# Performance work log

Hardware: AMD Instinct MI355X
Metric: run time of the kernel (lower is better)

Reference implementation:

```python
import jax, jax.numpy as jnp
import numpy as np

COMMITMENT_COST = 0.25
DECAY = 0.99
EPS = 1e-5
TOP_K = 3


def setup_inputs() -> dict:
    key = jax.random.key(0)
    k1, k2, k3, k4 = jax.random.split(key, 4)
    B, T, D, K = 16, 1024, 256, 4096
    return {
        "inputs": jax.random.normal(k1, (B, T, D), dtype=jnp.float32),
        "embedding_weight": jax.random.normal(k2, (K, D), dtype=jnp.float32),
        "ema_cluster_size": jax.random.uniform(k3, (K,), dtype=jnp.float32),
        "ema_w": jax.random.normal(k4, (K, D), dtype=jnp.float32),
    }


def reference(inputs, embedding_weight, ema_cluster_size, ema_w):
    B, T, D = inputs.shape
    K = embedding_weight.shape[0]
    flat = inputs.reshape(-1, D)  # [N, D], N = B*T
    N = flat.shape[0]

    dists = (jnp.sum(flat * flat, axis=1, keepdims=True)
             + jnp.sum(embedding_weight * embedding_weight, axis=1)
             - 2.0 * (flat @ embedding_weight.T))

    # top-k smallest distances
    _, idx = jax.lax.top_k(-dists, TOP_K)  # [N, k]

    # one-hot scatter encodings [N, K] (k ones per row)
    enc = jnp.zeros((N, K), dtype=flat.dtype).at[jnp.arange(N)[:, None], idx].set(1.0)

    # gather codebook vectors -> [B, T, k, D]
    quant = embedding_weight[idx].reshape(B, T, TOP_K, D)
    inp_rep = jnp.broadcast_to(inputs[:, :, None, :], (B, T, TOP_K, D))

    # EMA codebook update (training path)
    new_cs = ema_cluster_size * DECAY + (1.0 - DECAY) * enc.sum(axis=0)
    n = jnp.sum(new_cs)
    new_cs = (new_cs + EPS) / (n + K * EPS) * n
    dw = enc.T @ flat                                # [K, D]
    new_ema_w = ema_w * DECAY + (1.0 - DECAY) * dw
    updated_embeddings = new_ema_w / new_cs[:, None]

    # commitment loss with straight-through estimator
    e_latent_loss = jnp.mean((jax.lax.stop_gradient(quant) - inp_rep) ** 2)
    loss = COMMITMENT_COST * e_latent_loss
    quant_st = inp_rep + jax.lax.stop_gradient(quant - inp_rep)

    avg_probs = enc.mean(axis=0)
    perplexity = jnp.exp(-jnp.sum(avg_probs * jnp.log(avg_probs + 1e-10)))

    encoding_indices = idx.reshape(B, T, TOP_K)
    distances = dists.reshape(B, T, K)
    return (loss, quant_st, perplexity, avg_probs, encoding_indices, distances,
            new_cs, new_ema_w, updated_embeddings)
```

## Files before the change

### kernel.cpp

```cpp
#include <hip/hip_runtime.h>
#include <hip/hip_bf16.h>
#include <math.h>

#define N_ROWS 16384
#define DIM    256
#define KC     4096
#define TOPK   3
#define KSPLIT 768
#define TOTAL_E (N_ROWS * TOPK)
#define CHUNK 24

#define O_LOSS   0
#define O_QUANT  1
#define O_PERP   12582913
#define O_AVGP   12582914
#define O_IDX    12587010
#define O_DIST   12636162
#define O_NCS    79745026
#define O_NEMAW  79749122
#define O_UPD    80797698

typedef _Float16 h4_t __attribute__((ext_vector_type(4)));
typedef _Float16 h8_t __attribute__((ext_vector_type(8)));
typedef float    f4_t __attribute__((ext_vector_type(4)));

#define GLL(g, l) __builtin_amdgcn_global_load_lds( \
    (const __attribute__((address_space(1))) unsigned int*)(g), \
    (__attribute__((address_space(3))) unsigned int*)(l), 16, 0, 0)

__global__ __launch_bounds__(256) void rownorm_kernel(
    const float* __restrict__ X, float* __restrict__ out, int rows)
{
    int wave = threadIdx.x >> 6;
    int lane = threadIdx.x & 63;
    int row  = blockIdx.x * 4 + wave;
    if (row >= rows) return;
    float4 v = *(const float4*)&X[(size_t)row * DIM + lane * 4];
    float s = v.x*v.x + v.y*v.y + v.z*v.z + v.w*v.w;
    #pragma unroll
    for (int off = 32; off; off >>= 1) s += __shfl_down(s, off);
    if (lane == 0) out[row] = s;
}

__global__ __launch_bounds__(256) void convert_kernel(
    const float* __restrict__ X, _Float16* __restrict__ Q,
    int lo_off, int hi2_off)
{
    int wave = threadIdx.x >> 6;
    int lane = threadIdx.x & 63;
    int row  = blockIdx.x * 4 + wave;
    float4 v = *(const float4*)&X[(size_t)row * DIM + lane * 4];
    h4_t hi, lo;
    hi[0] = (_Float16)v.x; lo[0] = (_Float16)(v.x - (float)hi[0]);
    hi[1] = (_Float16)v.y; lo[1] = (_Float16)(v.y - (float)hi[1]);
    hi[2] = (_Float16)v.z; lo[2] = (_Float16)(v.z - (float)hi[2]);
    hi[3] = (_Float16)v.w; lo[3] = (_Float16)(v.w - (float)hi[3]);
    _Float16* q = Q + (size_t)row * KSPLIT + lane * 4;
    *(h4_t*)(q)           = hi;
    *(h4_t*)(q + hi2_off) = hi;
    *(h4_t*)(q + lo_off)  = lo;
}

__global__ __launch_bounds__(256) void gemm_dist_kernel(
    const _Float16* __restrict__ Aq,
    const _Float16* __restrict__ Bq,
    const float* __restrict__ xn,
    const float* __restrict__ en,
    float* __restrict__ dist)
{
    __shared__ _Float16 As[128 * 64];
    __shared__ _Float16 Bs[128 * 64];

    int bid = blockIdx.x;
    int swz = (bid & 7) * 512 + (bid >> 3);
    int m0 = (swz >> 5) * 128;
    int n0 = (swz & 31) * 128;

    const int tid = threadIdx.x;
    const int w = tid >> 6, l = tid & 63;
    const int wr = w >> 1, wc = w & 1;

    f4_t acc[4][4] = {};

    const int srow = l >> 3;
    const int scol = (l & 7) * 8;
    const _Float16* Abase = Aq + (size_t)m0 * KSPLIT;
    const _Float16* Bbase = Bq + (size_t)n0 * KSPLIT;

    for (int kt = 0; kt < KSPLIT; kt += 64) {
        #pragma unroll
        for (int i = 0; i < 4; i++) {
            int c = w * 4 + i;
            int rg = c * 8 + srow;
            GLL(Abase + (size_t)rg * KSPLIT + kt + scol, &As[c * 512]);
            GLL(Bbase + (size_t)rg * KSPLIT + kt + scol, &Bs[c * 512]);
        }
        __syncthreads();

        #pragma unroll
        for (int ks = 0; ks < 2; ks++) {
            h8_t a[4], b[4];
            #pragma unroll
            for (int mf = 0; mf < 4; mf++)
                a[mf] = *(const h8_t*)&As[(wr*64 + mf*16 + (l & 15)) * 64 + ks*32 + (l >> 4) * 8];
            #pragma unroll
            for (int nf = 0; nf < 4; nf++)
                b[nf] = *(const h8_t*)&Bs[(wc*64 + nf*16 + (l & 15)) * 64 + ks*32 + (l >> 4) * 8];
            #pragma unroll
            for (int mf = 0; mf < 4; mf++)
                #pragma unroll
                for (int nf = 0; nf < 4; nf++)
                    acc[mf][nf] = __builtin_amdgcn_mfma_f32_16x16x32_f16(
                        a[mf], b[nf], acc[mf][nf], 0, 0, 0);
        }
        __syncthreads();
    }

    const int cl = l & 15, rh = l >> 4;
    float ecv[4];
    #pragma unroll
    for (int nf = 0; nf < 4; nf++) ecv[nf] = en[n0 + wc*64 + nf*16 + cl];

    #pragma unroll
    for (int mf = 0; mf < 4; mf++) {
        int r0 = m0 + wr*64 + mf*16 + rh*4;
        float x0 = xn[r0], x1 = xn[r0+1], x2 = xn[r0+2], x3 = xn[r0+3];
        #pragma unroll
        for (int nf = 0; nf < 4; nf++) {
            int c = n0 + wc*64 + nf*16 + cl;
            float* dp = &dist[(size_t)r0 * KC + c];
            dp[0]           = x0 + ecv[nf] - 2.0f * acc[mf][nf][0];
            dp[(size_t)KC]  = x1 + ecv[nf] - 2.0f * acc[mf][nf][1];
            dp[(size_t)KC*2]= x2 + ecv[nf] - 2.0f * acc[mf][nf][2];
            dp[(size_t)KC*3]= x3 + ecv[nf] - 2.0f * acc[mf][nf][3];
        }
    }
}

__device__ __forceinline__ bool vi_lt(float v, int i, float u, int j)
{
    return (v < u) || (v == u && i < j);
}

__global__ __launch_bounds__(256) void top3_kernel(
    const float* __restrict__ dist, int* __restrict__ idxw,
    float* __restrict__ out_idx, float* __restrict__ counts,
    float* __restrict__ loss_part)
{
    __shared__ float blk_loss;
    if (threadIdx.x == 0) blk_loss = 0.0f;
    __syncthreads();

    int wave = threadIdx.x >> 6;
    int lane = threadIdx.x & 63;
    int row  = blockIdx.x * 4 + wave;
    const float* dr = dist + (size_t)row * KC;

    float v0 = INFINITY, v1 = INFINITY, v2 = INFINITY;
    int   i0 = 0x7fffffff, i1 = 0x7fffffff, i2 = 0x7fffffff;

    #pragma unroll 4
    for (int it = 0; it < 16; it++) {
        int c = (it * 64 + lane) * 4;
        float4 d = *(const float4*)&dr[c];
        float dv[4] = {d.x, d.y, d.z, d.w};
        #pragma unroll
        for (int q = 0; q < 4; q++) {
            float v = dv[q]; int ci = c + q;
            if (vi_lt(v, ci, v2, i2)) {
                v2 = v; i2 = ci;
                if (vi_lt(v2, i2, v1, i1)) { float tv = v1; int ti = i1; v1 = v2; i1 = i2; v2 = tv; i2 = ti; }
                if (vi_lt(v1, i1, v0, i0)) { float tv = v0; int ti = i0; v0 = v1; i0 = i1; v1 = tv; i1 = ti; }
            }
        }
    }

    #pragma unroll
    for (int off = 1; off < 64; off <<= 1) {
        float u0 = __shfl_xor(v0, off), u1 = __shfl_xor(v1, off), u2 = __shfl_xor(v2, off);
        int   j0 = __shfl_xor(i0, off), j1 = __shfl_xor(i1, off), j2 = __shfl_xor(i2, off);
        float av[3] = {v0, v1, v2}; int ai[3] = {i0, i1, i2};
        float bv[3] = {u0, u1, u2}; int bi[3] = {j0, j1, j2};
        float rv[3]; int ri[3];
        int p = 0, q = 0;
        #pragma unroll
        for (int t = 0; t < 3; t++) {
            bool ta = vi_lt(av[p], ai[p], bv[q], bi[q]);
            rv[t] = ta ? av[p] : bv[q];
            ri[t] = ta ? ai[p] : bi[q];
            p += ta ? 1 : 0; q += ta ? 0 : 1;
        }
        v0 = rv[0]; v1 = rv[1]; v2 = rv[2];
        i0 = ri[0]; i1 = ri[1]; i2 = ri[2];
    }

    if (lane == 0) {
        int base = row * TOPK;
        idxw[base + 0] = i0; idxw[base + 1] = i1; idxw[base + 2] = i2;
        out_idx[base + 0] = (float)i0;
        out_idx[base + 1] = (float)i1;
        out_idx[base + 2] = (float)i2;
        atomicAdd(&counts[i0], 1.0f);
        atomicAdd(&counts[i1], 1.0f);
        atomicAdd(&counts[i2], 1.0f);
        atomicAdd(&blk_loss, v0 + v1 + v2);
    }
    __syncthreads();
    if (threadIdx.x == 0) loss_part[blockIdx.x] = blk_loss;
}

__global__ __launch_bounds__(256) void quant_copy_kernel(
    const int* __restrict__ idxw, const float* __restrict__ E,
    float* __restrict__ quant_out)
{
    int wave = threadIdx.x >> 6;
    int lane = threadIdx.x & 63;
    int j = blockIdx.x * 4 + wave;
    int code = idxw[j];
    float4 v = *(const float4*)&E[(size_t)code * DIM + lane * 4];
    *(float4*)&quant_out[(size_t)j * DIM + lane * 4] = v;
}

__global__ __launch_bounds__(256) void kstage1_kernel(
    const float* __restrict__ counts, const float* __restrict__ ecs,
    float* __restrict__ avgp, float* __restrict__ scalars)
{
    int k = blockIdx.x * 256 + threadIdx.x;
    float cnt = counts[k];
    float pr = ecs[k] * 0.99f + 0.01f * cnt;
    float p = cnt * (1.0f / (float)N_ROWS);
    avgp[k] = p;
    float ent = p * logf(p + 1e-10f);
    int lane = threadIdx.x & 63;
    #pragma unroll
    for (int off = 32; off; off >>= 1) {
        pr  += __shfl_down(pr, off);
        ent += __shfl_down(ent, off);
    }
    if (lane == 0) {
        atomicAdd(&scalars[0], pr);
        atomicAdd(&scalars[2], ent);
    }
}

__global__ __launch_bounds__(256) void kstage2_kernel(
    const float* __restrict__ counts, const float* __restrict__ ecs,
    const float* __restrict__ scalars, float* __restrict__ ncs)
{
    int k = blockIdx.x * 256 + threadIdx.x;
    float pre = ecs[k] * 0.99f + 0.01f * counts[k];
    float nt = scalars[0];
    ncs[k] = (pre + 1e-5f) / (nt + (float)KC * 1e-5f) * nt;
}

__global__ __launch_bounds__(1024) void scan_kernel(
    const float* __restrict__ counts, int* __restrict__ offsets)
{
    __shared__ int lds[1024];
    int t = threadIdx.x;
    int c[4]; int s = 0;
    #pragma unroll
    for (int q = 0; q < 4; q++) { c[q] = (int)(counts[t * 4 + q] + 0.5f); s += c[q]; }
    lds[t] = s;
    __syncthreads();
    for (int off = 1; off < 1024; off <<= 1) {
        int v = (t >= off) ? lds[t - off] : 0;
        __syncthreads();
        lds[t] += v;
        __syncthreads();
    }
    int base = lds[t] - s;
    offsets[t * 4 + 0] = base;
    offsets[t * 4 + 1] = base + c[0];
    offsets[t * 4 + 2] = base + c[0] + c[1];
    offsets[t * 4 + 3] = base + c[0] + c[1] + c[2];
    if (t == 1023) offsets[4096] = lds[1023];
}

__global__ __launch_bounds__(256) void bucket_fill_kernel(
    const int* __restrict__ idxw, const int* __restrict__ offsets,
    int* __restrict__ fill, int* __restrict__ bucket_list)
{
    int j = blockIdx.x * 256 + threadIdx.x;
    int code = idxw[j];
    int pos = atomicAdd(&fill[code], 1);
    bucket_list[offsets[code] + pos] = (code << 14) | (j / 3);
}

__global__ __launch_bounds__(256) void codeacc_kernel(
    const int* __restrict__ bl, const float* __restrict__ flat,
    float* __restrict__ dw)
{
    int wave = threadIdx.x >> 6;
    int lane = threadIdx.x & 63;
    int chunk = blockIdx.x * 4 + wave;
    int beg = chunk * CHUNK;

    int ent[CHUNK];
    #pragma unroll
    for (int q = 0; q < CHUNK; q++) ent[q] = bl[beg + q];

    float4 acc = {0.0f, 0.0f, 0.0f, 0.0f};
    int prev = ent[0] >> 14;
    #pragma unroll
    for (int q = 0; q < CHUNK; q++) {
        int code = ent[q] >> 14;
        int n    = ent[q] & 0x3fff;
        if (code != prev) {
            float* p = &dw[(size_t)prev * DIM + lane * 4];
            atomicAdd(p + 0, acc.x); atomicAdd(p + 1, acc.y);
            atomicAdd(p + 2, acc.z); atomicAdd(p + 3, acc.w);
            acc.x = acc.y = acc.z = acc.w = 0.0f;
            prev = code;
        }
        float4 v = *(const float4*)&flat[(size_t)n * DIM + lane * 4];
        acc.x += v.x; acc.y += v.y; acc.z += v.z; acc.w += v.w;
    }
    float* p = &dw[(size_t)prev * DIM + lane * 4];
    atomicAdd(p + 0, acc.x); atomicAdd(p + 1, acc.y);
    atomicAdd(p + 2, acc.z); atomicAdd(p + 3, acc.w);
}

__global__ __launch_bounds__(256) void finalize_kernel(
    const float* __restrict__ dw, const float* __restrict__ emaw,
    const float* __restrict__ ncs, float* __restrict__ nemaw,
    float* __restrict__ upd)
{
    int wave = threadIdx.x >> 6;
    int lane = threadIdx.x & 63;
    int k = blockIdx.x * 4 + wave;
    size_t o = (size_t)k * DIM + lane * 4;
    float4 d = *(const float4*)&dw[o];
    float4 w = *(const float4*)&emaw[o];
    float4 nm;
    nm.x = 0.99f * w.x + 0.01f * d.x;
    nm.y = 0.99f * w.y + 0.01f * d.y;
    nm.z = 0.99f * w.z + 0.01f * d.z;
    nm.w = 0.99f * w.w + 0.01f * d.w;
    *(float4*)&nemaw[o] = nm;
    float inv = ncs[k];
    float4 u = {nm.x / inv, nm.y / inv, nm.z / inv, nm.w / inv};
    *(float4*)&upd[o] = u;
}

__global__ __launch_bounds__(1024) void loss_reduce_kernel(
    const float* __restrict__ lp, float* __restrict__ out)
{
    __shared__ float ls[16];
    int t = threadIdx.x;
    float s = lp[t] + lp[t + 1024] + lp[t + 2048] + lp[t + 3072];
    #pragma unroll
    for (int off = 32; off; off >>= 1) s += __shfl_down(s, off);
    if ((t & 63) == 0) ls[t >> 6] = s;
    __syncthreads();
    if (t == 0) {
        float tot = 0.0f;
        #pragma unroll
        for (int i = 0; i < 16; i++) tot += ls[i];
        out[O_LOSS] = 0.25f * tot / (float)(N_ROWS * TOPK * DIM);
    }
}

__global__ void final_kernel(const float* __restrict__ scalars, float* __restrict__ out)
{
    out[O_PERP] = expf(-scalars[2]);
}

extern "C" void kernel_launch(void* const* d_in, const int* in_sizes, int n_in,
                              void* d_out, int out_size, void* d_ws, size_t ws_size,
                              hipStream_t stream)
{
    const float* inputs = (const float*)d_in[0];
    const float* emb    = (const float*)d_in[1];
    const float* ecs    = (const float*)d_in[2];
    const float* emaw   = (const float*)d_in[3];
    float* out = (float*)d_out;
    char* ws = (char*)d_ws;

    int*   idxw        = (int*)ws;
    int*   bucket_list = (int*)(ws + 196608);
    float* counts      = (float*)(ws + 393216);
    int*   offsets     = (int*)(ws + 409600);
    int*   fill        = (int*)(ws + 430080);
    float* xn          = (float*)(ws + 446464);
    float* en          = (float*)(ws + 512000);
    float* scalars     = (float*)(ws + 528384);
    float* loss_part   = (float*)(ws + 528448);

    _Float16* Aq = (_Float16*)(out + 4);
    _Float16* Bq = (_Float16*)(out + 6291464);
    float*    dw = out + 8000000;

    hipMemsetAsync(counts, 0, KC * sizeof(float), stream);
    hipMemsetAsync(fill, 0, KC * sizeof(int), stream);
    hipMemsetAsync(scalars, 0, 8 * sizeof(float), stream);
    hipMemsetAsync(dw, 0, KC * DIM * sizeof(float), stream);

    convert_kernel<<<N_ROWS / 4, 256, 0, stream>>>(inputs, Aq, 512, 256);
    convert_kernel<<<KC / 4, 256, 0, stream>>>(emb, Bq, 256, 512);

    rownorm_kernel<<<N_ROWS / 4, 256, 0, stream>>>(inputs, xn, N_ROWS);
    rownorm_kernel<<<KC / 4, 256, 0, stream>>>(emb, en, KC);

    gemm_dist_kernel<<<(N_ROWS / 128) * (KC / 128), 256, 0, stream>>>(
        Aq, Bq, xn, en, out + O_DIST);

    top3_kernel<<<N_ROWS / 4, 256, 0, stream>>>(
        out + O_DIST, idxw, out + O_IDX, counts, loss_part);

    kstage1_kernel<<<KC / 256, 256, 0, stream>>>(counts, ecs, out + O_AVGP, scalars);
    kstage2_kernel<<<KC / 256, 256, 0, stream>>>(counts, ecs, scalars, out + O_NCS);
    scan_kernel<<<1, 1024, 0, stream>>>(counts, offsets);
    bucket_fill_kernel<<<(N_ROWS * TOPK) / 256, 256, 0, stream>>>(
        idxw, offsets, fill, bucket_list);

    codeacc_kernel<<<(TOTAL_E / CHUNK) / 4, 256, 0, stream>>>(
        bucket_list, inputs, dw);
    finalize_kernel<<<KC / 4, 256, 0, stream>>>(
        dw, emaw, out + O_NCS, out + O_NEMAW, out + O_UPD);

    quant_copy_kernel<<<(N_ROWS * TOPK) / 4, 256, 0, stream>>>(
        idxw, emb, out + O_QUANT);

    loss_reduce_kernel<<<1, 1024, 0, stream>>>(loss_part, out);
    final_kernel<<<1, 1, 0, stream>>>(scalars, out);
}
```

Baseline: 723.6 us.

## Fuse per-tile top-3 selection into distance GEMM epilogue and swizzle LDS

Computes a partial top-3 per row for each 128-column tile inside the GEMM epilogue. Partials are combined through shuffles and LDS, then written to a small partial buffer that a lightweight merge kernel reduces to the final top-3. This removes the full re-read of the 268 MB distance matrix by the old top3 kernel. It also adds an XOR swizzle to the LDS layout to reduce bank conflicts on fragment reads, at the cost of extra epilogue work and a scratch region carved out of the output buffer.

```diff
diff --git a/kernel.cpp b/kernel.cpp
--- a/kernel.cpp
+++ b/kernel.cpp
@@ -27,6 +27,32 @@
 #define GLL(g, l) __builtin_amdgcn_global_load_lds( \
     (const __attribute__((address_space(1))) unsigned int*)(g), \
     (__attribute__((address_space(3))) unsigned int*)(l), 16, 0, 0)
+
+__device__ __forceinline__ bool vi_lt(float v, int i, float u, int j)
+{
+    return (v < u) || (v == u && i < j);
+}
+
+__device__ __forceinline__ void ins3(float v, int i,
+    float& v0, int& i0, float& v1, int& i1, float& v2, int& i2)
+{
+    if (vi_lt(v, i, v2, i2)) {
+        v2 = v; i2 = i;
+        if (vi_lt(v2, i2, v1, i1)) { float tv=v1; int ti=i1; v1=v2; i1=i2; v2=tv; i2=ti; }
+        if (vi_lt(v1, i1, v0, i0)) { float tv=v0; int ti=i0; v0=v1; i0=i1; v1=tv; i1=ti; }
+    }
+}
+
+#define MERGE_SHFL(off) { \
+    float u0=__shfl_xor(v0,off), u1=__shfl_xor(v1,off), u2=__shfl_xor(v2,off); \
+    int   j0=__shfl_xor(i0,off), j1=__shfl_xor(i1,off), j2=__shfl_xor(i2,off); \
+    float av[3]={v0,v1,v2}; int ai[3]={i0,i1,i2}; \
+    float bv[3]={u0,u1,u2}; int bi[3]={j0,j1,j2}; \
+    float rv[3]; int ri[3]; int p=0,q=0; \
+    _Pragma("unroll") \
+    for (int t=0;t<3;t++){ bool ta=vi_lt(av[p],ai[p],bv[q],bi[q]); \
+      rv[t]=ta?av[p]:bv[q]; ri[t]=ta?ai[p]:bi[q]; p+=ta?1:0; q+=ta?0:1; } \
+    v0=rv[0];v1=rv[1];v2=rv[2];i0=ri[0];i1=ri[1];i2=ri[2]; }
 
 __global__ __launch_bounds__(256) void rownorm_kernel(
     const float* __restrict__ X, float* __restrict__ out, int rows)
@@ -66,7 +92,8 @@
     const _Float16* __restrict__ Bq,
     const float* __restrict__ xn,
     const float* __restrict__ en,
-    float* __restrict__ dist)
+    float* __restrict__ dist,
+    float2* __restrict__ part)
 {
     __shared__ _Float16 As[128 * 64];
     __shared__ _Float16 Bs[128 * 64];
@@ -83,7 +110,7 @@
     f4_t acc[4][4] = {};
 
     const int srow = l >> 3;
-    const int scol = (l & 7) * 8;
+    const int scol = ((l & 7) ^ srow) * 8;
     const _Float16* Abase = Aq + (size_t)m0 * KSPLIT;
     const _Float16* Bbase = Bq + (size_t)n0 * KSPLIT;
 
@@ -101,11 +128,17 @@
         for (int ks = 0; ks < 2; ks++) {
             h8_t a[4], b[4];
             #pragma unroll
-            for (int mf = 0; mf < 4; mf++)
-                a[mf] = *(const h8_t*)&As[(wr*64 + mf*16 + (l & 15)) * 64 + ks*32 + (l >> 4) * 8];
+            for (int mf = 0; mf < 4; mf++) {
+                int ra = wr*64 + mf*16 + (l & 15);
+                int ho = (ks*32 + (l >> 4) * 8) ^ ((ra & 7) * 8);
+                a[mf] = *(const h8_t*)&As[ra * 64 + ho];
+            }
             #pragma unroll
-            for (int nf = 0; nf < 4; nf++)
-                b[nf] = *(const h8_t*)&Bs[(wc*64 + nf*16 + (l & 15)) * 64 + ks*32 + (l >> 4) * 8];
+            for (int nf = 0; nf < 4; nf++) {
+                int rb = wc*64 + nf*16 + (l & 15);
+                int ho = (ks*32 + (l >> 4) * 8) ^ ((rb & 7) * 8);
+                b[nf] = *(const h8_t*)&Bs[rb * 64 + ho];
+            }
             #pragma unroll
             for (int mf = 0; mf < 4; mf++)
                 #pragma unroll
@@ -121,29 +154,62 @@
     #pragma unroll
     for (int nf = 0; nf < 4; nf++) ecv[nf] = en[n0 + wc*64 + nf*16 + cl];
 
+    float2* pt = (float2*)As;
+
     #pragma unroll
     for (int mf = 0; mf < 4; mf++) {
         int r0 = m0 + wr*64 + mf*16 + rh*4;
-        float x0 = xn[r0], x1 = xn[r0+1], x2 = xn[r0+2], x3 = xn[r0+3];
+        float xr[4] = {xn[r0], xn[r0+1], xn[r0+2], xn[r0+3]};
+        float dv[4][4];
         #pragma unroll
         for (int nf = 0; nf < 4; nf++) {
             int c = n0 + wc*64 + nf*16 + cl;
             float* dp = &dist[(size_t)r0 * KC + c];
-            dp[0]           = x0 + ecv[nf] - 2.0f * acc[mf][nf][0];
-            dp[(size_t)KC]  = x1 + ecv[nf] - 2.0f * acc[mf][nf][1];
-            dp[(size_t)KC*2]= x2 + ecv[nf] - 2.0f * acc[mf][nf][2];
-            dp[(size_t)KC*3]= x3 + ecv[nf] - 2.0f * acc[mf][nf][3];
+            #pragma unroll
+            for (int rg = 0; rg < 4; rg++) {
+                float d = xr[rg] + ecv[nf] - 2.0f * acc[mf][nf][rg];
+                dv[nf][rg] = d;
+                dp[(size_t)KC * rg] = d;
+            }
         }
-    }
-}
-
-__device__ __forceinline__ bool vi_lt(float v, int i, float u, int j)
-{
-    return (v < u) || (v == u && i < j);
-}
-
-__global__ __launch_bounds__(256) void top3_kernel(
-    const float* __restrict__ dist, int* __restrict__ idxw,
+        #pragma unroll
+        for (int rg = 0; rg < 4; rg++) {
+            float v0=INFINITY, v1=INFINITY, v2=INFINITY;
+            int   i0=0x7fffffff, i1=0x7fffffff, i2=0x7fffffff;
+            #pragma unroll
+            for (int nf = 0; nf < 4; nf++)
+                ins3(dv[nf][rg], n0 + wc*64 + nf*16 + cl, v0,i0,v1,i1,v2,i2);
+            MERGE_SHFL(1); MERGE_SHFL(2); MERGE_SHFL(4); MERGE_SHFL(8);
+            if (cl == 0) {
+                int rl = wr*64 + mf*16 + rh*4 + rg;
+                float2* q = &pt[(rl*2 + wc)*3];
+                q[0] = make_float2(v0, __int_as_float(i0));
+                q[1] = make_float2(v1, __int_as_float(i1));
+                q[2] = make_float2(v2, __int_as_float(i2));
+            }
+        }
+    }
+    __syncthreads();
+    if (tid < 128) {
+        float2 a0=pt[tid*6+0], a1=pt[tid*6+1], a2=pt[tid*6+2];
+        float2 b0=pt[tid*6+3], b1=pt[tid*6+4], b2=pt[tid*6+5];
+        float av[3]={a0.x,a1.x,a2.x};
+        int   ai[3]={__float_as_int(a0.y),__float_as_int(a1.y),__float_as_int(a2.y)};
+        float bv[3]={b0.x,b1.x,b2.x};
+        int   bi[3]={__float_as_int(b0.y),__float_as_int(b1.y),__float_as_int(b2.y)};
+        float rv[3]; int ri[3]; int p=0,q=0;
+        #pragma unroll
+        for (int t=0;t<3;t++){ bool ta=vi_lt(av[p],ai[p],bv[q],bi[q]);
+            rv[t]=ta?av[p]:bv[q]; ri[t]=ta?ai[p]:bi[q]; p+=ta?1:0; q+=ta?0:1; }
+        float2* dst = &part[((size_t)(m0 + tid) * 32 + (n0 >> 7)) * 3];
+        dst[0] = make_float2(rv[0], __int_as_float(ri[0]));
+        dst[1] = make_float2(rv[1], __int_as_float(ri[1]));
+        dst[2] = make_float2(rv[2], __int_as_float(ri[2]));
+    }
+}
+
+__global__ __launch_bounds__(256) void merge_top3_kernel(
+    const float2* __restrict__ part, int* __restrict__ idxw,
     float* __restrict__ out_idx, float* __restrict__ counts,
     float* __restrict__ loss_part)
 {
@@ -154,45 +220,20 @@
     int wave = threadIdx.x >> 6;
     int lane = threadIdx.x & 63;
     int row  = blockIdx.x * 4 + wave;
-    const float* dr = dist + (size_t)row * KC;
-
-    float v0 = INFINITY, v1 = INFINITY, v2 = INFINITY;
-    int   i0 = 0x7fffffff, i1 = 0x7fffffff, i2 = 0x7fffffff;
-
-    #pragma unroll 4
-    for (int it = 0; it < 16; it++) {
-        int c = (it * 64 + lane) * 4;
-        float4 d = *(const float4*)&dr[c];
-        float dv[4] = {d.x, d.y, d.z, d.w};
-        #pragma unroll
-        for (int q = 0; q < 4; q++) {
-            float v = dv[q]; int ci = c + q;
-            if (vi_lt(v, ci, v2, i2)) {
-                v2 = v; i2 = ci;
-                if (vi_lt(v2, i2, v1, i1)) { float tv = v1; int ti = i1; v1 = v2; i1 = i2; v2 = tv; i2 = ti; }
-                if (vi_lt(v1, i1, v0, i0)) { float tv = v0; int ti = i0; v0 = v1; i0 = i1; v1 = tv; i1 = ti; }
-            }
-        }
-    }
-
-    #pragma unroll
-    for (int off = 1; off < 64; off <<= 1) {
-        float u0 = __shfl_xor(v0, off), u1 = __shfl_xor(v1, off), u2 = __shfl_xor(v2, off);
-        int   j0 = __shfl_xor(i0, off), j1 = __shfl_xor(i1, off), j2 = __shfl_xor(i2, off);
-        float av[3] = {v0, v1, v2}; int ai[3] = {i0, i1, i2};
-        float bv[3] = {u0, u1, u2}; int bi[3] = {j0, j1, j2};
-        float rv[3]; int ri[3];
-        int p = 0, q = 0;
-        #pragma unroll
-        for (int t = 0; t < 3; t++) {
-            bool ta = vi_lt(av[p], ai[p], bv[q], bi[q]);
-            rv[t] = ta ? av[p] : bv[q];
-            ri[t] = ta ? ai[p] : bi[q];
-            p += ta ? 1 : 0; q += ta ? 0 : 1;
-        }
-        v0 = rv[0]; v1 = rv[1]; v2 = rv[2];
-        i0 = ri[0]; i1 = ri[1]; i2 = ri[2];
-    }
+    const float2* pr = part + (size_t)row * 96;
+
+    float v0=INFINITY, v1=INFINITY, v2=INFINITY;
+    int   i0=0x7fffffff, i1=0x7fffffff, i2=0x7fffffff;
+
+    float2 e0 = pr[lane];
+    ins3(e0.x, __float_as_int(e0.y), v0,i0,v1,i1,v2,i2);
+    if (lane < 32) {
+        float2 e1 = pr[64 + lane];
+        ins3(e1.x, __float_as_int(e1.y), v0,i0,v1,i1,v2,i2);
+    }
+
+    MERGE_SHFL(1); MERGE_SHFL(2); MERGE_SHFL(4);
+    MERGE_SHFL(8); MERGE_SHFL(16); MERGE_SHFL(32);
 
     if (lane == 0) {
         int base = row * TOPK;
@@ -387,9 +428,10 @@
     float* scalars     = (float*)(ws + 528384);
     float* loss_part   = (float*)(ws + 528448);
 
-    _Float16* Aq = (_Float16*)(out + 4);
-    _Float16* Bq = (_Float16*)(out + 6291464);
-    float*    dw = out + 8000000;
+    _Float16* Aq   = (_Float16*)(out + 4);
+    _Float16* Bq   = (_Float16*)(out + 6291464);
+    float*    dw   = out + 8000000;
+    float2*   part = (float2*)(out + 9100000);
 
     hipMemsetAsync(counts, 0, KC * sizeof(float), stream);
     hipMemsetAsync(fill, 0, KC * sizeof(int), stream);
@@ -403,10 +445,10 @@
     rownorm_kernel<<<KC / 4, 256, 0, stream>>>(emb, en, KC);
 
     gemm_dist_kernel<<<(N_ROWS / 128) * (KC / 128), 256, 0, stream>>>(
-        Aq, Bq, xn, en, out + O_DIST);
-
-    top3_kernel<<<N_ROWS / 4, 256, 0, stream>>>(
-        out + O_DIST, idxw, out + O_IDX, counts, loss_part);
+        Aq, Bq, xn, en, out + O_DIST, part);
+
+    merge_top3_kernel<<<N_ROWS / 4, 256, 0, stream>>>(
+        part, idxw, out + O_IDX, counts, loss_part);
 
     kstage1_kernel<<<KC / 256, 256, 0, stream>>>(counts, ecs, out + O_AVGP, scalars);
     kstage2_kernel<<<KC / 256, 256, 0, stream>>>(counts, ecs, scalars, out + O_NCS);
```

New measurement: 1.369 ms. 1.89x slower.
